# Kernel optimization log

Hardware: AMD Instinct MI355X
Metric: run time of the kernel (lower is better)

## Reference

```python
import jax, jax.numpy as jnp
import numpy as np

N, S, D, H = 32, 256, 1024, 1024


def setup_inputs() -> dict:
    key = jax.random.key(0)
    k1, k2, k3 = jax.random.split(key, 3)
    x = jax.random.normal(k1, (N, S, D), dtype=jnp.float32)
    mask = jnp.ones((N, S), dtype=jnp.float32)
    # Learned parameters (xavier-ish scale; original init_weights has a bug that
    weight_ih = jax.random.normal(k2, (8, D, H), dtype=jnp.float32) * (1.0 / np.sqrt(D))
    weight_hh = jax.random.normal(k3, (8, H, H), dtype=jnp.float32) * (1.0 / np.sqrt(H))
    bias = jnp.zeros((8, 1, H), dtype=jnp.float32)
    return {"x": x, "mask": mask, "weight_ih": weight_ih, "weight_hh": weight_hh, "bias": bias}


def _bilstm(x, mask, weight_ih, weight_hh, bias):
    n, s, d = x.shape
    h = weight_hh.shape[-1]
    # Precompute input contributions for all 8 gate/direction combos: [8,N,S,H]
    x_h = jnp.einsum('nsd,gdh->gnsh', x, weight_ih) + bias[:, None]
    xs_f = jnp.transpose(x_h[:4], (2, 0, 1, 3))          # [S,4,N,H] time-major fwd
    xs_b = jnp.transpose(x_h[4:], (2, 0, 1, 3))[::-1]    # [S,4,N,H] time-major bwd (reversed)
    m = mask[..., None]                                   # [N,S,1]
    mf = jnp.transpose(m, (1, 0, 2))                      # [S,N,1]
    mb = mf[::-1]
    Whh_f, Whh_b = weight_hh[:4], weight_hh[4:]
    h0 = jnp.zeros((n, h), x.dtype)

    def cell(hid, c, xg, Whh, mt):
        pre = xg + jnp.einsum('nh,ghk->gnk', hid, Whh)    # [4,N,H]
        f = jax.nn.sigmoid(pre[0])
        i = jax.nn.sigmoid(pre[1])
        o = jax.nn.sigmoid(pre[2])
        c = f * c + i * jnp.tanh(pre[3])                  # cell updates unmasked (as in torch)
        h_new = o * jnp.tanh(c)
        hid = jnp.where(mt == 0.0, hid, h_new)            # mask gates hidden only
        return hid, c

    def step(carry, xs):
        hf, cf, hb, cb = carry
        xf, xb, mtf, mtb = xs
        hf, cf = cell(hf, cf, xf, Whh_f, mtf)
        hb, cb = cell(hb, cb, xb, Whh_b, mtb)
        return (hf, cf, hb, cb), (hf, hb)

    _, (hs_f, hs_b) = jax.lax.scan(step, (h0, h0, h0, h0), (xs_f, xs_b, mf, mb))
    hs_f = jnp.transpose(hs_f, (1, 0, 2))                 # [N,S,H]
    hs_b = jnp.transpose(hs_b[::-1], (1, 0, 2))           # un-reverse backward states
    hidden_states = jnp.concatenate([hs_f, hs_b], axis=-1) * m
    final_state = jnp.concatenate([hs_f[:, -1, :], hs_b[:, 0, :]], axis=-1)
    return hidden_states, final_state


def reference(x, mask, weight_ih, weight_hh, bias):
    return _bilstm(x, mask, weight_ih, weight_hh, bias)
```

## Files before the change

kernel.cpp:

```cpp
#include <hip/hip_runtime.h>
#include <hip/hip_bf16.h>

using bf16 = __hip_bfloat16;
using bf16x8 = __attribute__((ext_vector_type(8))) short;
using f32x4  = __attribute__((ext_vector_type(4))) float;
typedef unsigned long long u64;

#define S_LEN 256
#define NBATCH 32
#define HDIM 1024
#define NBLK 256
#define SENT 0x7F7F7F7Fu
#define SENT64 0x7F7F7F7F7F7F7F7Full
#define GSTRIDE (8192ull * 1024ull)

__device__ __forceinline__ float fast_sig(float x) {
    return __builtin_amdgcn_rcpf(1.f + __expf(-x));
}
__device__ __forceinline__ float fast_tanh(float x) {
    return 1.f - 2.f * __builtin_amdgcn_rcpf(1.f + __expf(2.f * x));
}
__device__ __forceinline__ bool is_stale(u64 v) {
    return ((unsigned)v == SENT) || ((unsigned)(v >> 32) == SENT);
}

__global__ __launch_bounds__(256) void convert_x(const float* __restrict__ x,
                                                 bf16* __restrict__ xT) {
    const int p = blockIdx.x;
    const int n = p >> 8;
    const int s = p & 255;
    const float* src = x + (size_t)p * 1024;
    bf16* dst = xT + (size_t)(s * NBATCH + n) * 1024;
#pragma unroll
    for (int j = 0; j < 4; j++) {
        const int d = threadIdx.x + j * 256;
        dst[d] = (bf16)src[d];
    }
}

__global__ __launch_bounds__(256) void convert_transpose_1024(const float* __restrict__ in,
                                                              bf16* __restrict__ out) {
    __shared__ float t[32][33];
    const int g  = blockIdx.z;
    const float* A = in  + (size_t)g * 1024 * 1024;
    bf16*        B = out + (size_t)g * 1024 * 1024;
    const int c0 = blockIdx.x * 32;
    const int r0 = blockIdx.y * 32;
    const int tx = threadIdx.x, ty = threadIdx.y;
#pragma unroll
    for (int j = 0; j < 32; j += 8)
        t[ty + j][tx] = A[(size_t)(r0 + ty + j) * 1024 + c0 + tx];
    __syncthreads();
#pragma unroll
    for (int j = 0; j < 32; j += 8)
        B[(size_t)(c0 + ty + j) * 1024 + r0 + tx] = (bf16)t[tx][ty + j];
}

template <typename T>
__global__ __launch_bounds__(256) void xh_gemm(
        const bf16* __restrict__ xT,
        const bf16* __restrict__ wihT,
        const float* __restrict__ bias,
        T* __restrict__ xh) {
    __shared__ bf16 At[128 * 64];
    __shared__ bf16 Bt[128 * 64];
    const int g    = blockIdx.z;
    const int row0 = blockIdx.x * 128;
    const int col0 = blockIdx.y * 128;
    const int tid  = threadIdx.x;
    const int lane = tid & 63;
    const int wid  = tid >> 6;
    const int r16  = lane & 15;
    const int q    = lane >> 4;
    const int wr   = (wid >> 1) * 64;
    const int wc   = (wid & 1) * 64;
    const bf16* A = xT;
    const bf16* B = wihT + (size_t)g * 1024 * 1024;

    const f32x4 vzero = {0.f, 0.f, 0.f, 0.f};
    f32x4 acc[4][4];
#pragma unroll
    for (int m = 0; m < 4; m++)
#pragma unroll
        for (int n = 0; n < 4; n++) acc[m][n] = vzero;

    const int srow   = tid >> 3;
    const int skoff  = (tid & 7) * 8;
    const int schunk = tid & 7;

    for (int kt = 0; kt < 16; ++kt) {
#pragma unroll
        for (int inst = 0; inst < 4; inst++) {
            const int rowA = inst * 32 + srow;
            const int sdst = rowA * 64 + ((schunk ^ (rowA & 7)) << 3);
            bf16x8 va = *(const bf16x8*)(A + (size_t)(row0 + rowA) * 1024 + kt * 64 + skoff);
            *(bf16x8*)(At + sdst) = va;
            bf16x8 vb = *(const bf16x8*)(B + (size_t)(col0 + rowA) * 1024 + kt * 64 + skoff);
            *(bf16x8*)(Bt + sdst) = vb;
        }
        __syncthreads();
#pragma unroll
        for (int it = 0; it < 2; it++) {
            bf16x8 af[4], bfr[4];
#pragma unroll
            for (int m = 0; m < 4; m++) {
                const int arow = wr + m * 16 + r16;
                af[m] = *(const bf16x8*)(At + arow * 64 + ((((it << 2) | q) ^ (arow & 7)) << 3));
            }
#pragma unroll
            for (int n = 0; n < 4; n++) {
                const int brow = wc + n * 16 + r16;
                bfr[n] = *(const bf16x8*)(Bt + brow * 64 + ((((it << 2) | q) ^ (brow & 7)) << 3));
            }
#pragma unroll
            for (int m = 0; m < 4; m++)
#pragma unroll
                for (int n = 0; n < 4; n++)
                    acc[m][n] = __builtin_amdgcn_mfma_f32_16x16x32_bf16(af[m], bfr[n], acc[m][n], 0, 0, 0);
        }
        __syncthreads();
    }
    T* C = xh + (size_t)g * GSTRIDE;
    float bcol[4];
#pragma unroll
    for (int n = 0; n < 4; n++)
        bcol[n] = bias[g * 1024 + col0 + wc + n * 16 + r16];
#pragma unroll
    for (int m = 0; m < 4; m++)
#pragma unroll
        for (int n = 0; n < 4; n++)
#pragma unroll
            for (int j = 0; j < 4; j++)
                C[(size_t)(row0 + wr + m * 16 + q * 4 + j) * 1024 + col0 + wc + n * 16 + r16]
                    = (T)(acc[m][n][j] + bcol[n]);
}

template <typename T>
__global__ __launch_bounds__(1024, 4) void lstm_rec(
        const bf16* __restrict__ whhT,
        const T* __restrict__ xh,
        const float* __restrict__ mask,
        unsigned* __restrict__ hstate,
        unsigned* __restrict__ flags,
        float* __restrict__ out) {
    __shared__ float part[16 * 1024];

    const int bi    = blockIdx.x;
    const int xcd   = bi & 7;
    const int local = bi >> 3;
    const int dir   = xcd & 1;
    const int ng    = xcd >> 1;
    const int col0  = local * 32;
    const int tid   = threadIdx.x;
    const int w     = tid >> 6;
    const int lane  = tid & 63;
    const int r16   = lane & 15;
    const int q     = lane >> 4;
    const int kbase = w * 64;

    bf16x8 bw[8][2];
#pragma unroll
    for (int c = 0; c < 8; c++) {
        const size_t rowoff =
            ((size_t)((dir * 4 + (c >> 1)) * 1024 + col0 + (c & 1) * 16 + r16)) * 1024
            + kbase + q * 8;
#pragma unroll
        for (int it = 0; it < 2; it++)
            bw[c][it] = *(const bf16x8*)(whhT + rowoff + it * 32);
    }

    const int un = tid >> 5;
    const int uc = tid & 31;
    float creg = 0.f, hreg = 0.f;

    const unsigned* fp = flags + xcd * 32 + (lane & 31);
    const f32x4 vzero = {0.f, 0.f, 0.f, 0.f};

    for (int t = 0; t < S_LEN; ++t) {
        const int s_idx = dir ? (S_LEN - 1 - t) : t;

        float xf = 0.f, xi = 0.f, xo = 0.f, xg = 0.f, mt = 0.f;
        if (tid < 256) {
            const size_t xb = ((size_t)(dir * 4) * GSTRIDE)
                            + ((size_t)(s_idx * 32 + ng * 8 + un)) * 1024 + col0 + uc;
            xf = (float)xh[xb];
            xi = (float)xh[xb + GSTRIDE];
            xo = (float)xh[xb + 2 * GSTRIDE];
            xg = (float)xh[xb + 3 * GSTRIDE];
            mt = mask[(ng * 8 + un) * S_LEN + s_idx];
        }

        {
            int fg = 0;
            while (true) {
                const unsigned fl = __hip_atomic_load(fp,
                    __ATOMIC_RELAXED, __HIP_MEMORY_SCOPE_AGENT);
                if (__all((int)fl >= t) || ++fg > (1 << 20)) break;
            }
        }

        u64 hq[4];
        hq[0] = 0; hq[1] = 0; hq[2] = 0; hq[3] = 0;
        const u64* Hq = (const u64*)hstate
            + ((size_t)(((t & 3) * 8 + xcd) * 8 + r16)) * 256
            + (kbase >> 2) + q * 2;
        if (r16 < 8) {
            hq[0] = __hip_atomic_load(Hq,     __ATOMIC_RELAXED, __HIP_MEMORY_SCOPE_AGENT);
            hq[1] = __hip_atomic_load(Hq + 1, __ATOMIC_RELAXED, __HIP_MEMORY_SCOPE_AGENT);
            hq[2] = __hip_atomic_load(Hq + 8, __ATOMIC_RELAXED, __HIP_MEMORY_SCOPE_AGENT);
            hq[3] = __hip_atomic_load(Hq + 9, __ATOMIC_RELAXED, __HIP_MEMORY_SCOPE_AGENT);
            int guard = 0;
            while (true) {
                const bool st = is_stale(hq[0]) | is_stale(hq[1])
                              | is_stale(hq[2]) | is_stale(hq[3]);
                if (!st || ++guard > 8192) break;
                if (is_stale(hq[0]))
                    hq[0] = __hip_atomic_load(Hq,     __ATOMIC_RELAXED, __HIP_MEMORY_SCOPE_AGENT);
                if (is_stale(hq[1]))
                    hq[1] = __hip_atomic_load(Hq + 1, __ATOMIC_RELAXED, __HIP_MEMORY_SCOPE_AGENT);
                if (is_stale(hq[2]))
                    hq[2] = __hip_atomic_load(Hq + 8, __ATOMIC_RELAXED, __HIP_MEMORY_SCOPE_AGENT);
                if (is_stale(hq[3]))
                    hq[3] = __hip_atomic_load(Hq + 9, __ATOMIC_RELAXED, __HIP_MEMORY_SCOPE_AGENT);
            }
        }

        union { u64 qv[2]; bf16x8 v; } av0, av1;
        av0.qv[0] = hq[0]; av0.qv[1] = hq[1];
        av1.qv[0] = hq[2]; av1.qv[1] = hq[3];
#pragma unroll
        for (int c = 0; c < 8; c++) {
            f32x4 a = vzero;
            a = __builtin_amdgcn_mfma_f32_16x16x32_bf16(av0.v, bw[c][0], a, 0, 0, 0);
            a = __builtin_amdgcn_mfma_f32_16x16x32_bf16(av1.v, bw[c][1], a, 0, 0, 0);
            if (lane < 32) {
#pragma unroll
                for (int j = 0; j < 4; j++)
                    part[w * 1024 + (q * 4 + j) * 128 + (c >> 1) * 32 + (c & 1) * 16 + r16]
                        = a[j];
            }
        }
        __syncthreads();

        if (tid < 256) {
            if ((uc & 3) == 0) {
                u64* rdst = (u64*)hstate
                    + ((size_t)((((t + 2) & 3) * 8 + xcd) * 8 + un)) * 256
                    + ((col0 + uc) >> 2);
                __hip_atomic_store(rdst, SENT64, __ATOMIC_RELAXED, __HIP_MEMORY_SCOPE_AGENT);
            }
            float pf = xf, pi = xi, po = xo, pg = xg;
#pragma unroll
            for (int ww = 0; ww < 16; ww++) {
                const float* p = part + ww * 1024 + un * 128;
                pf += p[uc];
                pi += p[32 + uc];
                po += p[64 + uc];
                pg += p[96 + uc];
            }
            const float f  = fast_sig(pf);
            const float i  = fast_sig(pi);
            const float o  = fast_sig(po);
            const float ct = fast_tanh(pg);
            creg = f * creg + i * ct;
            const float hnew = o * fast_tanh(creg);
            const float hcar = (mt == 0.f) ? hreg : hnew;
            hreg = hcar;
            union { bf16 b; unsigned short u; } cv;
            cv.b = (bf16)hcar;
            const unsigned mine  = cv.u;
            const unsigned other = (unsigned)__shfl_xor((int)mine, 1);
            const unsigned pair  = mine | (other << 16);
            const unsigned pair2 = (unsigned)__shfl_xor((int)pair, 2);
            if ((uc & 3) == 0) {
                u64* dst = (u64*)hstate
                    + ((size_t)((((t + 1) & 3) * 8 + xcd) * 8 + un)) * 256
                    + ((col0 + uc) >> 2);
                __hip_atomic_store(dst, (u64)pair | ((u64)pair2 << 32),
                                   __ATOMIC_RELAXED, __HIP_MEMORY_SCOPE_AGENT);
            }
            out[((size_t)((ng * 8 + un) * S_LEN + s_idx)) * 2048 + dir * 1024 + col0 + uc]
                = hcar * mt;
            if (t == S_LEN - 1)
                out[(size_t)NBATCH * S_LEN * 2048 + (ng * 8 + un) * 2048 + dir * 1024 + col0 + uc]
                    = hcar;
        }
        __syncthreads();

        if (tid == 0)
            __hip_atomic_store(flags + xcd * 32 + local, (unsigned)(t + 1),
                               __ATOMIC_RELAXED, __HIP_MEMORY_SCOPE_AGENT);
    }
}

__global__ __launch_bounds__(1024) void lstm_persistent(
        const bf16* __restrict__ xT,
        const bf16* __restrict__ wihT,
        const bf16* __restrict__ whhT,
        const float* __restrict__ mask,
        const float* __restrict__ bias,
        unsigned* __restrict__ hbuf,
        float* __restrict__ out) {
    __shared__ float part[16 * 1024];

    const int bi   = blockIdx.x;
    const int dir  = bi & 1;
    const int col0 = ((bi >> 1) & 127) << 3;
    const int tid  = threadIdx.x;
    const int w    = tid >> 6;
    const int lane = tid & 63;
    const int r    = lane & 15;
    const int q    = lane >> 4;
    const int kbase = w * 64 + q * 8;

    bf16x8 bx[2][2], bh[2][2];
#pragma unroll
    for (int gp = 0; gp < 2; gp++) {
        const int gate = gp * 2 + (r >> 3);
        const size_t rowoff = ((size_t)((dir * 4 + gate) * 1024 + col0 + (r & 7))) * 1024 + kbase;
#pragma unroll
        for (int it = 0; it < 2; it++) {
            bx[gp][it] = *(const bf16x8*)(wihT + rowoff + it * 32);
            bh[gp][it] = *(const bf16x8*)(whhT + rowoff + it * 32);
        }
    }

    const int un = tid >> 3;
    const int uc = tid & 7;
    float creg = 0.f, hreg = 0.f;
    float b0 = 0.f, b1 = 0.f, b2 = 0.f, b3 = 0.f;
    if (tid < 256) {
        const int gb = (dir * 4) * 1024 + col0 + uc;
        b0 = bias[gb];
        b1 = bias[gb + 1024];
        b2 = bias[gb + 2048];
        b3 = bias[gb + 3072];
    }
    const int rx = (un & 7) * 4;

    const f32x4 vzero = {0.f, 0.f, 0.f, 0.f};
    f32x4 accA[2][2], accB[2][2];
#pragma unroll
    for (int mh = 0; mh < 2; mh++) { accB[mh][0] = vzero; accB[mh][1] = vzero; }

    {
        const int s_id = dir ? (S_LEN - 1) : 0;
        const bf16* Ax = xT + (size_t)s_id * NBATCH * HDIM + kbase;
#pragma unroll
        for (int mh = 0; mh < 2; mh++) {
            accA[mh][0] = vzero; accA[mh][1] = vzero;
#pragma unroll
            for (int it = 0; it < 2; it++) {
                bf16x8 a = *(const bf16x8*)(Ax + (size_t)(mh * 16 + r) * HDIM + it * 32);
                accA[mh][0] = __builtin_amdgcn_mfma_f32_16x16x32_bf16(a, bx[0][it], accA[mh][0], 0, 0, 0);
                accA[mh][1] = __builtin_amdgcn_mfma_f32_16x16x32_bf16(a, bx[1][it], accA[mh][1], 0, 0, 0);
            }
        }
    }

    for (int t = 0; t < S_LEN; ++t) {
        const int s_idx = dir ? (S_LEN - 1 - t) : t;
        float mt = 0.f;
        if (tid < 256) mt = mask[un * S_LEN + s_idx];

        const u64* Hp = (const u64*)hbuf
                      + ((size_t)((t & 3) * 2 + dir) * NBATCH) * 256 + (kbase >> 2);
        u64 hv[2][2][2];
#pragma unroll
        for (int mh = 0; mh < 2; mh++)
#pragma unroll
            for (int it = 0; it < 2; it++)
#pragma unroll
                for (int j = 0; j < 2; j++)
                    hv[mh][it][j] = __hip_atomic_load(
                        Hp + (size_t)(mh * 16 + r) * 256 + it * 8 + j,
                        __ATOMIC_RELAXED, __HIP_MEMORY_SCOPE_AGENT);

        if (t + 1 < S_LEN) {
            const int s_id = dir ? (S_LEN - 2 - t) : (t + 1);
            const bf16* Ax = xT + (size_t)s_id * NBATCH * HDIM + kbase;
#pragma unroll
            for (int mh = 0; mh < 2; mh++) {
                accB[mh][0] = vzero; accB[mh][1] = vzero;
#pragma unroll
                for (int it = 0; it < 2; it++) {
                    bf16x8 a = *(const bf16x8*)(Ax + (size_t)(mh * 16 + r) * HDIM + it * 32);
                    accB[mh][0] = __builtin_amdgcn_mfma_f32_16x16x32_bf16(a, bx[0][it], accB[mh][0], 0, 0, 0);
                    accB[mh][1] = __builtin_amdgcn_mfma_f32_16x16x32_bf16(a, bx[1][it], accB[mh][1], 0, 0, 0);
                }
            }
        }

        {
            int guard = 0;
            while (true) {
                bool stale = false;
#pragma unroll
                for (int mh = 0; mh < 2; mh++)
#pragma unroll
                    for (int it = 0; it < 2; it++)
#pragma unroll
                        for (int j = 0; j < 2; j++)
                            stale |= is_stale(hv[mh][it][j]);
                if (!stale || ++guard > 8192) break;
#pragma unroll
                for (int mh = 0; mh < 2; mh++)
#pragma unroll
                    for (int it = 0; it < 2; it++)
#pragma unroll
                        for (int j = 0; j < 2; j++)
                            if (is_stale(hv[mh][it][j]))
                                hv[mh][it][j] = __hip_atomic_load(
                                    Hp + (size_t)(mh * 16 + r) * 256 + it * 8 + j,
                                    __ATOMIC_RELAXED, __HIP_MEMORY_SCOPE_AGENT);
            }
        }

#pragma unroll
        for (int mh = 0; mh < 2; mh++)
#pragma unroll
            for (int it = 0; it < 2; it++) {
                union { u64 qv[2]; bf16x8 v; } av;
                av.qv[0] = hv[mh][it][0];
                av.qv[1] = hv[mh][it][1];
                accA[mh][0] = __builtin_amdgcn_mfma_f32_16x16x32_bf16(av.v, bh[0][it], accA[mh][0], 0, 0, 0);
                accA[mh][1] = __builtin_amdgcn_mfma_f32_16x16x32_bf16(av.v, bh[1][it], accA[mh][1], 0, 0, 0);
            }

        {
            float* slab = part + w * 1024;
#pragma unroll
            for (int mh = 0; mh < 2; mh++)
#pragma unroll
                for (int gp = 0; gp < 2; gp++)
#pragma unroll
                    for (int rr = 0; rr < 4; rr++) {
                        const int row = mh * 16 + q * 4 + rr;
                        const int pc = (gp * 16 + r) ^ ((row & 7) * 4);
                        slab[row * 32 + pc] = accA[mh][gp][rr];
                    }
        }
#pragma unroll
        for (int mh = 0; mh < 2; mh++) { accA[mh][0] = accB[mh][0]; accA[mh][1] = accB[mh][1]; }
        __syncthreads();

        if (tid < 256) {
            if ((uc & 3) == 0) {
                u64* rdst = (u64*)hbuf
                    + ((size_t)(((t + 2) & 3) * 2 + dir) * NBATCH + un) * 256
                    + ((col0 + uc) >> 2);
                __hip_atomic_store(rdst, SENT64, __ATOMIC_RELAXED, __HIP_MEMORY_SCOPE_AGENT);
            }
            float pf = b0, pi = b1, po = b2, pg = b3;
            const int rowbase = un * 32;
#pragma unroll
            for (int ww = 0; ww < 16; ww++) {
                const float* rowp = part + ww * 1024 + rowbase;
                pf += rowp[(0  + uc) ^ rx];
                pi += rowp[(8  + uc) ^ rx];
                po += rowp[(16 + uc) ^ rx];
                pg += rowp[(24 + uc) ^ rx];
            }
            const float f  = fast_sig(pf);
            const float i  = fast_sig(pi);
            const float o  = fast_sig(po);
            const float ct = fast_tanh(pg);
            creg = f * creg + i * ct;
            const float hnew = o * fast_tanh(creg);
            const float hcar = (mt == 0.f) ? hreg : hnew;
            hreg = hcar;
            union { bf16 b; unsigned short u; } cv;
            cv.b = (bf16)hcar;
            const unsigned mine  = cv.u;
            const unsigned other = (unsigned)__shfl_xor((int)mine, 1);
            const unsigned pair  = mine | (other << 16);
            const unsigned pair2 = (unsigned)__shfl_xor((int)pair, 2);
            if ((uc & 3) == 0) {
                u64* dst = (u64*)hbuf
                    + ((size_t)(((t + 1) & 3) * 2 + dir) * NBATCH + un) * 256
                    + ((col0 + uc) >> 2);
                __hip_atomic_store(dst, (u64)pair | ((u64)pair2 << 32),
                                   __ATOMIC_RELAXED, __HIP_MEMORY_SCOPE_AGENT);
            }
            out[((size_t)(un * S_LEN + s_idx)) * 2048 + dir * 1024 + col0 + uc] = hcar * mt;
            if (t == S_LEN - 1)
                out[(size_t)NBATCH * S_LEN * 2048 + un * 2048 + dir * 1024 + col0 + uc] = hcar;
        }
        __syncthreads();
    }
}

extern "C" void kernel_launch(void* const* d_in, const int* in_sizes, int n_in,
                              void* d_out, int out_size, void* d_ws, size_t ws_size,
                              hipStream_t stream) {
    const float* x    = (const float*)d_in[0];
    const float* mask = (const float*)d_in[1];
    const float* wih  = (const float*)d_in[2];
    const float* whh  = (const float*)d_in[3];
    const float* bias = (const float*)d_in[4];
    float* out = (float*)d_out;

    char* ws = (char*)d_ws;
    bf16* xT   = (bf16*)(ws);
    bf16* wihT = (bf16*)(ws + 16777216);
    bf16* whhT = (bf16*)(ws + 33554432);

    convert_x<<<NBATCH * S_LEN, 256, 0, stream>>>(x, xT);
    dim3 tb(32, 8);
    convert_transpose_1024<<<dim3(32, 32, 8), tb, 0, stream>>>(wih, wihT);
    convert_transpose_1024<<<dim3(32, 32, 8), tb, 0, stream>>>(whh, whhT);

    if (ws_size >= 319292416ull) {
        float*    xh     = (float*)(ws + 50331648);
        unsigned* hstate = (unsigned*)(ws + 318767104);
        unsigned* flags  = (unsigned*)(ws + 318767104 + 524288);
        hipMemsetAsync((char*)hstate, 0x00, 131072, stream);
        hipMemsetAsync((char*)hstate + 131072, 0x7F, 393216, stream);
        hipMemsetAsync((char*)flags, 0x00, 1024, stream);
        xh_gemm<float><<<dim3(64, 8, 8), 256, 0, stream>>>(xT, wihT, bias, xh);
        lstm_rec<float><<<256, 1024, 0, stream>>>(whhT, xh, mask, hstate, flags, out);
    } else if (ws_size >= 185074688ull) {
        bf16*     xh     = (bf16*)(ws + 50331648);
        unsigned* hstate = (unsigned*)(ws + 184549376);
        unsigned* flags  = (unsigned*)(ws + 184549376 + 524288);
        hipMemsetAsync((char*)hstate, 0x00, 131072, stream);
        hipMemsetAsync((char*)hstate + 131072, 0x7F, 393216, stream);
        hipMemsetAsync((char*)flags, 0x00, 1024, stream);
        xh_gemm<bf16><<<dim3(64, 8, 8), 256, 0, stream>>>(xT, wihT, bias, xh);
        lstm_rec<bf16><<<256, 1024, 0, stream>>>(whhT, xh, mask, hstate, flags, out);
    } else {
        unsigned* hbuf = (unsigned*)(ws + 50331648);
        hipMemsetAsync((char*)hbuf, 0x00, 131072, stream);
        hipMemsetAsync((char*)hbuf + 131072, 0x7F, 393216, stream);
        lstm_persistent<<<NBLK, 1024, 0, stream>>>(xT, wihT, whhT, mask, bias,
                                                   hbuf, out);
    }
}
```

Before: 1.200 ms.

## Pad step flags to cache lines, prefetch next-step inputs, publish flag before output writes

Each per-block step flag now sits on its own 128-byte line instead of being packed densely, and a block no longer polls its own flag. The next timestep's input projections and mask are loaded during the current step, overlapping them with the hidden-state wait. The flag store is moved ahead of the global output writes so dependent blocks are released sooner. This raises workspace size thresholds and adds register pressure for the prefetched values. If the larger workspace is not available, the kernel falls back to a different path.

```diff
diff --git a/kernel.cpp b/kernel.cpp
--- a/kernel.cpp
+++ b/kernel.cpp
@@ -173,29 +173,31 @@
     const int uc = tid & 31;
     float creg = 0.f, hreg = 0.f;
 
-    const unsigned* fp = flags + xcd * 32 + (lane & 31);
+    const unsigned* fp = flags + (((size_t)xcd * 32 + (lane & 31)) << 5);
+    const bool ownflag = (lane & 31) == local;
     const f32x4 vzero = {0.f, 0.f, 0.f, 0.f};
+
+    float xf = 0.f, xi = 0.f, xo = 0.f, xg = 0.f, mt = 0.f;
+    if (tid < 256) {
+        const int s0 = dir ? (S_LEN - 1) : 0;
+        const size_t xb = ((size_t)(dir * 4) * GSTRIDE)
+                        + ((size_t)(s0 * 32 + ng * 8 + un)) * 1024 + col0 + uc;
+        xf = (float)xh[xb];
+        xi = (float)xh[xb + GSTRIDE];
+        xo = (float)xh[xb + 2 * GSTRIDE];
+        xg = (float)xh[xb + 3 * GSTRIDE];
+        mt = mask[(ng * 8 + un) * S_LEN + s0];
+    }
 
     for (int t = 0; t < S_LEN; ++t) {
         const int s_idx = dir ? (S_LEN - 1 - t) : t;
-
-        float xf = 0.f, xi = 0.f, xo = 0.f, xg = 0.f, mt = 0.f;
-        if (tid < 256) {
-            const size_t xb = ((size_t)(dir * 4) * GSTRIDE)
-                            + ((size_t)(s_idx * 32 + ng * 8 + un)) * 1024 + col0 + uc;
-            xf = (float)xh[xb];
-            xi = (float)xh[xb + GSTRIDE];
-            xo = (float)xh[xb + 2 * GSTRIDE];
-            xg = (float)xh[xb + 3 * GSTRIDE];
-            mt = mask[(ng * 8 + un) * S_LEN + s_idx];
-        }
 
         {
             int fg = 0;
             while (true) {
                 const unsigned fl = __hip_atomic_load(fp,
                     __ATOMIC_RELAXED, __HIP_MEMORY_SCOPE_AGENT);
-                if (__all((int)fl >= t) || ++fg > (1 << 20)) break;
+                if (__all(ownflag || ((int)fl >= t)) || ++fg > (1 << 20)) break;
             }
         }
 
@@ -209,6 +211,21 @@
             hq[1] = __hip_atomic_load(Hq + 1, __ATOMIC_RELAXED, __HIP_MEMORY_SCOPE_AGENT);
             hq[2] = __hip_atomic_load(Hq + 8, __ATOMIC_RELAXED, __HIP_MEMORY_SCOPE_AGENT);
             hq[3] = __hip_atomic_load(Hq + 9, __ATOMIC_RELAXED, __HIP_MEMORY_SCOPE_AGENT);
+        }
+
+        float nxf = 0.f, nxi = 0.f, nxo = 0.f, nxg = 0.f, nmt = 0.f;
+        if (t + 1 < S_LEN && tid < 256) {
+            const int s_nx = dir ? (S_LEN - 2 - t) : (t + 1);
+            const size_t xb = ((size_t)(dir * 4) * GSTRIDE)
+                            + ((size_t)(s_nx * 32 + ng * 8 + un)) * 1024 + col0 + uc;
+            nxf = (float)xh[xb];
+            nxi = (float)xh[xb + GSTRIDE];
+            nxo = (float)xh[xb + 2 * GSTRIDE];
+            nxg = (float)xh[xb + 3 * GSTRIDE];
+            nmt = mask[(ng * 8 + un) * S_LEN + s_nx];
+        }
+
+        if (r16 < 8) {
             int guard = 0;
             while (true) {
                 const bool st = is_stale(hq[0]) | is_stale(hq[1])
@@ -242,6 +259,7 @@
         }
         __syncthreads();
 
+        float hcar = 0.f;
         if (tid < 256) {
             if ((uc & 3) == 0) {
                 u64* rdst = (u64*)hstate
@@ -264,7 +282,7 @@
             const float ct = fast_tanh(pg);
             creg = f * creg + i * ct;
             const float hnew = o * fast_tanh(creg);
-            const float hcar = (mt == 0.f) ? hreg : hnew;
+            hcar = (mt == 0.f) ? hreg : hnew;
             hreg = hcar;
             union { bf16 b; unsigned short u; } cv;
             cv.b = (bf16)hcar;
@@ -279,17 +297,23 @@
                 __hip_atomic_store(dst, (u64)pair | ((u64)pair2 << 32),
                                    __ATOMIC_RELAXED, __HIP_MEMORY_SCOPE_AGENT);
             }
+        }
+        __syncthreads();
+
+        if (tid == 0)
+            __hip_atomic_store(flags + (((size_t)xcd * 32 + local) << 5),
+                               (unsigned)(t + 1),
+                               __ATOMIC_RELAXED, __HIP_MEMORY_SCOPE_AGENT);
+
+        if (tid < 256) {
             out[((size_t)((ng * 8 + un) * S_LEN + s_idx)) * 2048 + dir * 1024 + col0 + uc]
                 = hcar * mt;
             if (t == S_LEN - 1)
                 out[(size_t)NBATCH * S_LEN * 2048 + (ng * 8 + un) * 2048 + dir * 1024 + col0 + uc]
                     = hcar;
         }
-        __syncthreads();
-
-        if (tid == 0)
-            __hip_atomic_store(flags + xcd * 32 + local, (unsigned)(t + 1),
-                               __ATOMIC_RELAXED, __HIP_MEMORY_SCOPE_AGENT);
+
+        xf = nxf; xi = nxi; xo = nxo; xg = nxg; mt = nmt;
     }
 }
 
@@ -510,22 +534,22 @@
     convert_transpose_1024<<<dim3(32, 32, 8), tb, 0, stream>>>(wih, wihT);
     convert_transpose_1024<<<dim3(32, 32, 8), tb, 0, stream>>>(whh, whhT);
 
-    if (ws_size >= 319292416ull) {
+    if (ws_size >= 319324160ull) {
         float*    xh     = (float*)(ws + 50331648);
         unsigned* hstate = (unsigned*)(ws + 318767104);
         unsigned* flags  = (unsigned*)(ws + 318767104 + 524288);
         hipMemsetAsync((char*)hstate, 0x00, 131072, stream);
         hipMemsetAsync((char*)hstate + 131072, 0x7F, 393216, stream);
-        hipMemsetAsync((char*)flags, 0x00, 1024, stream);
+        hipMemsetAsync((char*)flags, 0x00, 32768, stream);
         xh_gemm<float><<<dim3(64, 8, 8), 256, 0, stream>>>(xT, wihT, bias, xh);
         lstm_rec<float><<<256, 1024, 0, stream>>>(whhT, xh, mask, hstate, flags, out);
-    } else if (ws_size >= 185074688ull) {
+    } else if (ws_size >= 185106432ull) {
         bf16*     xh     = (bf16*)(ws + 50331648);
         unsigned* hstate = (unsigned*)(ws + 184549376);
         unsigned* flags  = (unsigned*)(ws + 184549376 + 524288);
         hipMemsetAsync((char*)hstate, 0x00, 131072, stream);
         hipMemsetAsync((char*)hstate + 131072, 0x7F, 393216, stream);
-        hipMemsetAsync((char*)flags, 0x00, 1024, stream);
+        hipMemsetAsync((char*)flags, 0x00, 32768, stream);
         xh_gemm<bf16><<<dim3(64, 8, 8), 256, 0, stream>>>(xT, wihT, bias, xh);
         lstm_rec<bf16><<<256, 1024, 0, stream>>>(whhT, xh, mask, hstate, flags, out);
     } else {
```

Result: slower. 1.291 ms (+7.6%).
